# Kernel optimization log

Hardware: AMD Instinct MI355X
Metric: run time of the kernel (lower is better)

The kernel has to match this reference:

```python
import jax, jax.numpy as jnp
import numpy as np

B = 4096
FEATURES = 4608 + 4608 + 8 + 1  # 9225
LSTM = 512
R = FEATURES / LSTM
D1 = int(FEATURES / R ** (1.0 / 3.0))
D2 = int(FEATURES / R ** (2.0 / 3.0))
ACTION_SHAPES = (64, 64, 64, 64, 64, 64, 64, 64)


def setup_inputs() -> dict:
    key = jax.random.key(0)
    ks = jax.random.split(key, 32)
    s = 0.02
    inp = {
        "actualCanvasFeatures": jax.random.normal(ks[0], (B, 4608), jnp.float32),
        "objectiveCanvasFeatures": jax.random.normal(ks[1], (B, 4608), jnp.float32),
        "last_action": jax.random.uniform(ks[2], (B, 8), jnp.float32),
        "episode_percentage": 0,
        # encoder MLP
        "W1": jax.random.normal(ks[3], (FEATURES, D1), jnp.float32) * s,
        "b1": jnp.zeros((D1,), jnp.float32),
        "W2": jax.random.normal(ks[4], (D1, D2), jnp.float32) * s,
        "b2": jnp.zeros((D2,), jnp.float32),
        "W3": jax.random.normal(ks[5], (D2, LSTM), jnp.float32) * s,
        "b3": jnp.zeros((LSTM,), jnp.float32),
        # LSTM (torch gate order i,f,g,o)
        "Wih": jax.random.normal(ks[6], (4 * LSTM, LSTM), jnp.float32) * s,
        "Whh": jax.random.normal(ks[7], (4 * LSTM, LSTM), jnp.float32) * s,
        "bih": jnp.zeros((4 * LSTM,), jnp.float32),
        "bhh": jnp.zeros((4 * LSTM,), jnp.float32),
        "h0": jnp.zeros((B, LSTM), jnp.float32),
        "c0": jnp.zeros((B, LSTM), jnp.float32),
        # decoder
        "dW1": jax.random.normal(ks[8], (LSTM, LSTM // 2), jnp.float32) * s,
        "db1": jnp.zeros((LSTM // 2,), jnp.float32),
        "headWs": tuple(jax.random.normal(ks[9 + i], (LSTM // 2, a), jnp.float32) * s
                        for i, a in enumerate(ACTION_SHAPES)),
        "headbs": tuple(jnp.zeros((a,), jnp.float32) for a in ACTION_SHAPES),
        "dWo": jax.random.normal(ks[20], (LSTM + 1, LSTM), jnp.float32) * s,
        "dbo": jnp.zeros((LSTM,), jnp.float32),
    }
    return inp


def reference(actualCanvasFeatures, objectiveCanvasFeatures, last_action,
              episode_percentage, W1, b1, W2, b2, W3, b3, Wih, Whh, bih, bhh,
              h0, c0, dW1, db1, headWs, headbs, dWo, dbo):
    b = actualCanvasFeatures.shape[0]
    ep = jnp.full((b, 1), episode_percentage, dtype=jnp.float32)
    feats = jnp.concatenate(
        [actualCanvasFeatures, objectiveCanvasFeatures, last_action, ep], axis=1)
    # encoder MLP (dropout is eval-mode identity)
    x = jax.nn.relu(feats @ W1 + b1)
    x = jax.nn.relu(x @ W2 + b2)
    x = jax.nn.relu(x @ W3 + b3)
    # single-step LSTM cell, torch gate order i,f,g,o
    gates = x @ Wih.T + bih + h0 @ Whh.T + bhh
    i, f, g, o = jnp.split(gates, 4, axis=1)
    c = jax.nn.sigmoid(f) * c0 + jax.nn.sigmoid(i) * jnp.tanh(g)
    z = jax.nn.sigmoid(o) * jnp.tanh(c)  # seed
    key = jax.random.key(42)
    actions = []
    log_probabilities = jnp.zeros((b,), jnp.float32)
    entropy = jnp.float32(0.0)
    for Wk, bk in zip(headWs, headbs):
        z1 = jax.nn.relu(z @ dW1 + db1)
        logits = z1 @ Wk + bk
        logp = jax.nn.log_softmax(logits, axis=1)
        probs = jnp.exp(logp)
        key, sk = jax.random.split(key)
        act = jax.random.categorical(sk, logits, axis=1)  # [b] int
        actions.append(act.astype(jnp.float32))
        entropy = entropy + jnp.sum(-jnp.sum(probs * logp, axis=1))
        log_probabilities = log_probabilities + jnp.take_along_axis(
            logp, act[:, None], axis=1)[:, 0]
        z = jax.nn.relu(
            jnp.concatenate([z, act.astype(jnp.float32)[:, None]], axis=1) @ dWo + dbo)
    action = jnp.stack(actions, axis=1)  # [b, n_sub_actions]
    return action, entropy, log_probabilities
```

## Files before the change

### kernel.cpp

```cpp
#include <hip/hip_runtime.h>
#include <cstdint>
#include <cstring>

typedef _Float16 f16;
typedef _Float16 f16x8 __attribute__((ext_vector_type(8)));
typedef float f32x4 __attribute__((ext_vector_type(4)));

static constexpr int kPartitionable = 1;

__host__ __device__ inline void tf2x32(uint32_t k0, uint32_t k1,
                                       uint32_t x0, uint32_t x1,
                                       uint32_t& o0, uint32_t& o1) {
  uint32_t ks[3] = {k0, k1, k0 ^ k1 ^ 0x1BD11BDAu};
  uint32_t v0 = x0 + ks[0], v1 = x1 + ks[1];
  const int r0[4] = {13, 15, 26, 6};
  const int r1[4] = {17, 29, 16, 24};
  for (int g = 0; g < 5; ++g) {
    const int* rr = (g & 1) ? r1 : r0;
    for (int j = 0; j < 4; ++j) {
      v0 += v1;
      v1 = (v1 << rr[j]) | (v1 >> (32 - rr[j]));
      v1 ^= v0;
    }
    v0 += ks[(g + 1) % 3];
    v1 += ks[(g + 2) % 3] + (uint32_t)(g + 1);
  }
  o0 = v0; o1 = v1;
}

template <int BM, int BN>
__global__ __launch_bounds__(256, 2) void gemm_split(
    const f16* __restrict__ Ah, const f16* __restrict__ Al, int lda,
    const f16* __restrict__ Bh, const f16* __restrict__ Bl, int ldb,
    int K,
    const float* __restrict__ bias1, const float* __restrict__ bias2,
    int nReal, int relu, int writeF32,
    float* __restrict__ outF, f16* __restrict__ outH, f16* __restrict__ outL,
    int ldo) {
  constexpr int BK = 64;
  constexpr int TM = BM / 32;
  constexpr int TN = BN / 32;
  static_assert(BM == BN, "square tiles only");
  __shared__ f16 sAh[BM * BK];
  __shared__ f16 sAl[BM * BK];
  __shared__ f16 sBh[BN * BK];
  __shared__ f16 sBl[BN * BK];

  const int tid = threadIdx.x;
  const int wave = tid >> 6;
  const int lane = tid & 63;
  const int wm = wave & 1, wn = wave >> 1;
  const int m0 = blockIdx.x * BM;
  const int n0 = blockIdx.y * BN;

  f32x4 acc[TM][TN];
  const f32x4 zero = {0.f, 0.f, 0.f, 0.f};
#pragma unroll
  for (int i = 0; i < TM; ++i)
#pragma unroll
    for (int j = 0; j < TN; ++j) acc[i][j] = zero;

  const f16* src;
  f16* dst;
  int ld, base;
  if (wave == 0)      { src = Ah; dst = sAh; ld = lda; base = m0; }
  else if (wave == 1) { src = Al; dst = sAl; ld = lda; base = m0; }
  else if (wave == 2) { src = Bh; dst = sBh; ld = ldb; base = n0; }
  else                { src = Bl; dst = sBl; ld = ldb; base = n0; }
  constexpr int NITER = (BM * 8) / 64;

  for (int k0 = 0; k0 < K; k0 += BK) {
    __syncthreads();
#pragma unroll
    for (int j = 0; j < NITER; ++j) {
      int c = j * 64 + lane;
      int row = c >> 3, col = c & 7;
      const uint4* g = (const uint4*)(src + (size_t)(base + row) * ld + k0) + col;
      uint4 v = *g;
      ((uint4*)dst)[c] = v;
    }
    __syncthreads();
#pragma unroll
    for (int kk = 0; kk < BK; kk += 32) {
      const int fr = lane & 15;
      const int q8 = (lane >> 4) * 8;
      f16x8 aH[TM], aL[TM], bH[TN], bL[TN];
#pragma unroll
      for (int i = 0; i < TM; ++i) {
        int off = (wm * (BM / 2) + i * 16 + fr) * BK + kk + q8;
        aH[i] = *(const f16x8*)&sAh[off];
        aL[i] = *(const f16x8*)&sAl[off];
      }
#pragma unroll
      for (int j = 0; j < TN; ++j) {
        int off = (wn * (BN / 2) + j * 16 + fr) * BK + kk + q8;
        bH[j] = *(const f16x8*)&sBh[off];
        bL[j] = *(const f16x8*)&sBl[off];
      }
#pragma unroll
      for (int i = 0; i < TM; ++i)
#pragma unroll
        for (int j = 0; j < TN; ++j) {
          acc[i][j] = __builtin_amdgcn_mfma_f32_16x16x32_f16(aH[i], bH[j], acc[i][j], 0, 0, 0);
          acc[i][j] = __builtin_amdgcn_mfma_f32_16x16x32_f16(aH[i], bL[j], acc[i][j], 0, 0, 0);
          acc[i][j] = __builtin_amdgcn_mfma_f32_16x16x32_f16(aL[i], bH[j], acc[i][j], 0, 0, 0);
        }
    }
  }
  const int rq = lane >> 4, cl = lane & 15;
#pragma unroll
  for (int i = 0; i < TM; ++i)
#pragma unroll
    for (int j = 0; j < TN; ++j)
#pragma unroll
      for (int r = 0; r < 4; ++r) {
        int row = m0 + wm * (BM / 2) + i * 16 + rq * 4 + r;
        int col = n0 + wn * (BN / 2) + j * 16 + cl;
        float v = acc[i][j][r];
        if (col < nReal) {
          if (bias1) v += bias1[col];
          if (bias2) v += bias2[col];
          if (relu) v = fmaxf(v, 0.f);
        } else {
          v = 0.f;
        }
        size_t o = (size_t)row * ldo + col;
        if (writeF32) {
          outF[o] = v;
        } else {
          f16 h = (f16)v;
          outH[o] = h;
          outL[o] = (f16)(v - (float)h);
        }
      }
}

__global__ void conv_feats(const float* __restrict__ A, const float* __restrict__ O,
                           const float* __restrict__ LA, const int* __restrict__ EP,
                           f16* __restrict__ H, f16* __restrict__ L) {
  uint32_t idx = blockIdx.x * 256u + threadIdx.x;
  const uint32_t total = 4096u * 9280u;
  if (idx >= total) return;
  uint32_t b = idx / 9280u, c = idx - b * 9280u;
  float v;
  if (c < 4608u) v = A[(size_t)b * 4608 + c];
  else if (c < 9216u) v = O[(size_t)b * 4608 + (c - 4608u)];
  else if (c < 9224u) v = LA[(size_t)b * 8 + (c - 9216u)];
  else if (c == 9224u) v = (float)EP[0];
  else v = 0.f;
  f16 h = (f16)v;
  H[idx] = h;
  L[idx] = (f16)(v - (float)h);
}

__global__ void convT_kernel(const float* __restrict__ W, int Kreal, int Nreal,
                             f16* __restrict__ BtH, f16* __restrict__ BtL, int Kpad) {
  __shared__ float tile[32][33];
  int k0 = blockIdx.x * 32, n0 = blockIdx.y * 32;
  int tx = threadIdx.x, ty = threadIdx.y;
  for (int r = 0; r < 32; r += 8) {
    int k = k0 + ty + r, n = n0 + tx;
    float v = (k < Kreal && n < Nreal) ? W[(size_t)k * Nreal + n] : 0.f;
    tile[ty + r][tx] = v;
  }
  __syncthreads();
  for (int r = 0; r < 32; r += 8) {
    int n = n0 + ty + r, k = k0 + tx;
    float v = tile[tx][ty + r];
    size_t o = (size_t)n * Kpad + k;
    f16 h = (f16)v;
    BtH[o] = h;
    BtL[o] = (f16)(v - (float)h);
  }
}

__global__ void conv_lstmB(const float* __restrict__ Wih, const float* __restrict__ Whh,
                           f16* __restrict__ H, f16* __restrict__ L) {
  uint32_t idx = blockIdx.x * 256u + threadIdx.x;
  uint32_t n = idx >> 10, k = idx & 1023u;
  float v = (k < 512u) ? Wih[(size_t)n * 512 + k] : Whh[(size_t)n * 512 + (k - 512u)];
  f16 h = (f16)v;
  H[idx] = h;
  L[idx] = (f16)(v - (float)h);
}

__global__ void conv_h0(const float* __restrict__ h0, f16* __restrict__ H, f16* __restrict__ L) {
  uint32_t idx = blockIdx.x * 256u + threadIdx.x;
  uint32_t b = idx >> 9, j = idx & 511u;
  float v = h0[idx];
  size_t o = (size_t)b * 1024 + 512 + j;
  f16 h = (f16)v;
  H[o] = h;
  L[o] = (f16)(v - (float)h);
}

__global__ void lstm_pointwise(const float* __restrict__ gates, const float* __restrict__ c0,
                               f16* __restrict__ zH, f16* __restrict__ zL) {
  uint32_t idx = blockIdx.x * 256u + threadIdx.x;
  uint32_t b = idx >> 9, n = idx & 511u;
  const float* g = gates + (size_t)b * 2048;
  float gi = g[n], gf = g[512 + n], gg = g[1024 + n], go = g[1536 + n];
  float si = 1.f / (1.f + expf(-gi));
  float sf = 1.f / (1.f + expf(-gf));
  float so = 1.f / (1.f + expf(-go));
  float c = sf * c0[idx] + si * tanhf(gg);
  float z = so * tanhf(c);
  size_t o = (size_t)b * 576 + n;
  f16 h = (f16)z;
  zH[o] = h;
  zL[o] = (f16)(z - (float)h);
}

__global__ void init_ws(f16* zAH, f16* zAL, f16* zBH, f16* zBL,
                        float* wsLogp, float* wsEnt) {
  uint32_t idx = blockIdx.x * 256u + threadIdx.x;
  if (idx < 4096u * 63u) {
    uint32_t b = idx / 63u, c = 513u + idx - b * 63u;
    size_t o = (size_t)b * 576 + c;
    zAH[o] = (f16)0.f; zAL[o] = (f16)0.f; zBH[o] = (f16)0.f; zBL[o] = (f16)0.f;
  }
  if (idx < 4096u) wsLogp[idx] = 0.f;
  if (idx == 0) *wsEnt = 0.f;
}

__device__ inline double shfl_xor_dbl(double v, int m) {
  union { double d; int i[2]; } u;
  u.d = v;
  u.i[0] = __shfl_xor(u.i[0], m);
  u.i[1] = __shfl_xor(u.i[1], m);
  return u.d;
}

__global__ void sample_head(const float* __restrict__ logits,
                            uint32_t sk0, uint32_t sk1, int head, int partitionable,
                            float* __restrict__ outAct,
                            f16* __restrict__ zH, f16* __restrict__ zL,
                            float* __restrict__ wsLogp, float* __restrict__ wsEnt) {
  int wave = threadIdx.x >> 6, lane = threadIdx.x & 63;
  int b = blockIdx.x * 4 + wave;
  float l = logits[(size_t)b * 128 + lane];

  uint32_t i = (uint32_t)b * 64u + (uint32_t)lane;
  uint32_t bits;
  if (partitionable) {
    uint32_t o0, o1;
    tf2x32(sk0, sk1, 0u, i, o0, o1);
    bits = o0 ^ o1;
  } else {
    const uint32_t H = 131072u;
    uint32_t c0, c1, o0, o1;
    int pick;
    if (i < H) { c0 = i; c1 = i + H; pick = 0; }
    else       { c0 = i - H; c1 = i; pick = 1; }
    tf2x32(sk0, sk1, c0, c1, o0, o1);
    bits = pick ? o1 : o0;
  }
  uint32_t ub = (bits >> 9) | 0x3f800000u;
  float u;
  __builtin_memcpy(&u, &ub, 4);
  u -= 1.0f;
  if (u == 0.0f) u = 1.17549435e-38f;
  double gum = -log(-log((double)u));
  double s = (double)l + gum;

  int bi = lane;
  double bv = s;
#pragma unroll
  for (int off = 1; off < 64; off <<= 1) {
    double ov = shfl_xor_dbl(bv, off);
    int oi = __shfl_xor(bi, off);
    if (ov > bv || (ov == bv && oi < bi)) { bv = ov; bi = oi; }
  }
  int act = bi;

  float m = l;
#pragma unroll
  for (int off = 1; off < 64; off <<= 1) m = fmaxf(m, __shfl_xor(m, off));
  float e = expf(l - m);
  float S = e, D = e * l;
#pragma unroll
  for (int off = 1; off < 64; off <<= 1) {
    S += __shfl_xor(S, off);
    D += __shfl_xor(D, off);
  }
  float M = m + logf(S);
  float Hrow = M - D / S;
  float l_act = __shfl(l, act);

  if (lane == 0) {
    outAct[(size_t)b * 8 + head] = (float)act;
    wsLogp[b] += (l_act - M);
    size_t zo = (size_t)b * 576 + 512;
    zH[zo] = (f16)act;
    zL[zo] = (f16)0.f;
  }
  __shared__ float hs[4];
  if (lane == 0) hs[wave] = Hrow;
  __syncthreads();
  if (threadIdx.x == 0) atomicAdd(wsEnt, hs[0] + hs[1] + hs[2] + hs[3]);
}

__global__ void finalize_out(const float* __restrict__ wsEnt, const float* __restrict__ wsLogp,
                             float* __restrict__ out) {
  uint32_t idx = blockIdx.x * 256u + threadIdx.x;
  if (idx == 0) out[32768] = *wsEnt;
  if (idx < 4096u) out[32769 + idx] = wsLogp[idx];
}

extern "C" void kernel_launch(void* const* d_in, const int* in_sizes, int n_in,
                              void* d_out, int out_size, void* d_ws, size_t ws_size,
                              hipStream_t stream) {
  (void)in_sizes; (void)out_size; (void)ws_size;
  const float* actual = (const float*)d_in[0];
  const float* object = (const float*)d_in[1];
  const float* lastA = (const float*)d_in[2];
  const int* ep = (const int*)d_in[3];
  const float* W1 = (const float*)d_in[4];
  const float* b1 = (const float*)d_in[5];
  const float* W2 = (const float*)d_in[6];
  const float* b2 = (const float*)d_in[7];
  const float* W3 = (const float*)d_in[8];
  const float* b3 = (const float*)d_in[9];
  const float* Wih = (const float*)d_in[10];
  const float* Whh = (const float*)d_in[11];
  const float* bih = (const float*)d_in[12];
  const float* bhh = (const float*)d_in[13];
  const float* h0 = (const float*)d_in[14];
  const float* c0 = (const float*)d_in[15];
  const float* dW1 = (const float*)d_in[16];
  const float* db1 = (const float*)d_in[17];
  const float* headW[8];
  const float* headb[8];
  const float *dWo, *dbo;
  if (n_in >= 36) {
    for (int h = 0; h < 8; ++h) headW[h] = (const float*)d_in[18 + h];
    for (int h = 0; h < 8; ++h) headb[h] = (const float*)d_in[26 + h];
    dWo = (const float*)d_in[34];
    dbo = (const float*)d_in[35];
  } else {
    const float* hw = (const float*)d_in[18];
    const float* hb = (const float*)d_in[19];
    for (int h = 0; h < 8; ++h) { headW[h] = hw + (size_t)h * 256 * 64; headb[h] = hb + (size_t)h * 64; }
    dWo = (const float*)d_in[20];
    dbo = (const float*)d_in[21];
  }

  constexpr int Bq = 4096;
  constexpr int K1 = 9280, N1 = 3584, N1r = 3518;
  constexpr int K2 = 3584, N2 = 1408, N2r = 1342;
  constexpr int K3 = 1408, N3 = 512;
  constexpr int KL = 1024, NL = 2048;
  constexpr int KD1 = 512, ND1 = 256;
  constexpr int KH = 256, NHp = 128;
  constexpr int KDO = 576, NDO = 512;

  uint8_t* w = (uint8_t*)d_ws;
  size_t off = 0;
  auto alloc = [&](size_t bytes) -> void* {
    off = (off + 1023) & ~(size_t)1023;
    void* p = w + off;
    off += bytes;
    return p;
  };
  f16* A1h = (f16*)alloc((size_t)Bq * K1 * 2);
  f16* A1l = (f16*)alloc((size_t)Bq * K1 * 2);
  size_t fixedReuseEnd = off;
  f16* Bt1h = (f16*)alloc((size_t)N1 * K1 * 2);
  f16* Bt1l = (f16*)alloc((size_t)N1 * K1 * 2);
  f16* x1h = (f16*)alloc((size_t)Bq * K2 * 2);
  f16* x1l = (f16*)alloc((size_t)Bq * K2 * 2);
  f16* Bt2h = (f16*)alloc((size_t)N2 * K2 * 2);
  f16* Bt2l = (f16*)alloc((size_t)N2 * K2 * 2);
  size_t poff = 0;
  auto palloc = [&](size_t bytes) -> void* {
    poff = (poff + 1023) & ~(size_t)1023;
    void* p = w + poff;
    poff += bytes;
    return p;
  };
  f16* x2h = (f16*)palloc((size_t)Bq * K3 * 2);
  f16* x2l = (f16*)palloc((size_t)Bq * K3 * 2);
  f16* Bt3h = (f16*)palloc((size_t)N3 * K3 * 2);
  f16* Bt3l = (f16*)palloc((size_t)N3 * K3 * 2);
  f16* ALh = (f16*)palloc((size_t)Bq * KL * 2);
  f16* ALl = (f16*)palloc((size_t)Bq * KL * 2);
  f16* BLh = (f16*)palloc((size_t)NL * KL * 2);
  f16* BLl = (f16*)palloc((size_t)NL * KL * 2);
  float* gates = (float*)palloc((size_t)Bq * NL * 4);
  f16* zAH = (f16*)palloc((size_t)Bq * 576 * 2);
  f16* zAL = (f16*)palloc((size_t)Bq * 576 * 2);
  f16* zBH = (f16*)palloc((size_t)Bq * 576 * 2);
  f16* zBL = (f16*)palloc((size_t)Bq * 576 * 2);
  f16* Btd1h = (f16*)palloc((size_t)ND1 * KD1 * 2);
  f16* Btd1l = (f16*)palloc((size_t)ND1 * KD1 * 2);
  f16* z1h = (f16*)palloc((size_t)Bq * ND1 * 2);
  f16* z1l = (f16*)palloc((size_t)Bq * ND1 * 2);
  f16* Bthh = (f16*)palloc((size_t)8 * NHp * KH * 2);
  f16* Bthl = (f16*)palloc((size_t)8 * NHp * KH * 2);
  float* logitsF = (float*)palloc((size_t)Bq * 128 * 4);
  f16* Btdoh = (f16*)palloc((size_t)NDO * KDO * 2);
  f16* Btdol = (f16*)palloc((size_t)NDO * KDO * 2);
  float* wsLogp = (float*)palloc((size_t)Bq * 4);
  float* wsEnt = (float*)palloc(64);
  (void)fixedReuseEnd;

  uint32_t k0 = 0u, k1 = 42u;
  uint32_t sk[8][2];
  for (int h = 0; h < 8; ++h) {
    if (kPartitionable) {
      uint32_t a0, a1, b0v, b1v;
      tf2x32(k0, k1, 0u, 0u, a0, a1);
      tf2x32(k0, k1, 0u, 1u, b0v, b1v);
      sk[h][0] = b0v; sk[h][1] = b1v;
      k0 = a0; k1 = a1;
    } else {
      uint32_t a0, a1, b0v, b1v;
      tf2x32(k0, k1, 0u, 2u, a0, a1);
      tf2x32(k0, k1, 1u, 3u, b0v, b1v);
      sk[h][0] = a1; sk[h][1] = b1v;
      k0 = a0; k1 = b0v;
    }
  }

  dim3 blk(256);
  dim3 tblk(32, 8);

  conv_feats<<<(4096u * 9280u + 255) / 256, blk, 0, stream>>>(actual, object, lastA, ep, A1h, A1l);
  convT_kernel<<<dim3(K1 / 32, N1 / 32), tblk, 0, stream>>>(W1, 9225, 3518, Bt1h, Bt1l, K1);
  convT_kernel<<<dim3(K2 / 32, N2 / 32), tblk, 0, stream>>>(W2, 3518, 1342, Bt2h, Bt2l, K2);

  gemm_split<128, 128><<<dim3(Bq / 128, N1 / 128), blk, 0, stream>>>(
      A1h, A1l, K1, Bt1h, Bt1l, K1, K1, b1, nullptr, N1r, 1, 0, nullptr, x1h, x1l, K2);

  init_ws<<<(4096u * 63u + 255) / 256, blk, 0, stream>>>(zAH, zAL, zBH, zBL, wsLogp, wsEnt);
  convT_kernel<<<dim3(K3 / 32, N3 / 32), tblk, 0, stream>>>(W3, 1342, 512, Bt3h, Bt3l, K3);
  conv_lstmB<<<(2048u * 1024u) / 256, blk, 0, stream>>>(Wih, Whh, BLh, BLl);
  conv_h0<<<(4096u * 512u) / 256, blk, 0, stream>>>(h0, ALh, ALl);
  convT_kernel<<<dim3(KD1 / 32, ND1 / 32), tblk, 0, stream>>>(dW1, 512, 256, Btd1h, Btd1l, KD1);
  convT_kernel<<<dim3(KDO / 32, NDO / 32), tblk, 0, stream>>>(dWo, 513, 512, Btdoh, Btdol, KDO);
  for (int h = 0; h < 8; ++h)
    convT_kernel<<<dim3(KH / 32, NHp / 32), tblk, 0, stream>>>(
        headW[h], 256, 64, Bthh + (size_t)h * NHp * KH, Bthl + (size_t)h * NHp * KH, KH);

  gemm_split<128, 128><<<dim3(Bq / 128, N2 / 128), blk, 0, stream>>>(
      x1h, x1l, K2, Bt2h, Bt2l, K2, K2, b2, nullptr, N2r, 1, 0, nullptr, x2h, x2l, K3);
  gemm_split<128, 128><<<dim3(Bq / 128, N3 / 128), blk, 0, stream>>>(
      x2h, x2l, K3, Bt3h, Bt3l, K3, K3, b3, nullptr, N3, 1, 0, nullptr, ALh, ALl, KL);
  gemm_split<128, 128><<<dim3(Bq / 128, NL / 128), blk, 0, stream>>>(
      ALh, ALl, KL, BLh, BLl, KL, KL, bih, bhh, NL, 0, 1, gates, nullptr, nullptr, NL);
  lstm_pointwise<<<(4096u * 512u) / 256, blk, 0, stream>>>(gates, c0, zAH, zAL);

  for (int h = 0; h < 8; ++h) {
    f16* curH = (h & 1) ? zBH : zAH;
    f16* curL = (h & 1) ? zBL : zAL;
    f16* nxtH = (h & 1) ? zAH : zBH;
    f16* nxtL = (h & 1) ? zAL : zBL;
    gemm_split<64, 64><<<dim3(Bq / 64, ND1 / 64), blk, 0, stream>>>(
        curH, curL, 576, Btd1h, Btd1l, KD1, KD1, db1, nullptr, ND1, 1, 0, nullptr, z1h, z1l, ND1);
    gemm_split<64, 64><<<dim3(Bq / 64, NHp / 64), blk, 0, stream>>>(
        z1h, z1l, ND1, Bthh + (size_t)h * NHp * KH, Bthl + (size_t)h * NHp * KH, KH, KH,
        headb[h], nullptr, 64, 0, 1, logitsF, nullptr, nullptr, 128);
    sample_head<<<Bq / 4, blk, 0, stream>>>(logitsF, sk[h][0], sk[h][1], h, kPartitionable,
                                            (float*)d_out, curH, curL, wsLogp, wsEnt);
    gemm_split<64, 64><<<dim3(Bq / 64, NDO / 64), blk, 0, stream>>>(
        curH, curL, 576, Btdoh, Btdol, KDO, KDO, dbo, nullptr, NDO, 1, 0, nullptr, nxtH, nxtL, 576);
  }
  finalize_out<<<(4097 + 255) / 256, blk, 0, stream>>>(wsEnt, wsLogp, (float*)d_out);
}
```

Baseline: 2.311 ms.

## Use direct global-to-LDS loads with XOR-swizzled layouts and trim head padding

Replaces the register-staged global→LDS copy in the split-fp16 GEMM with the global_load_lds builtin. All producer kernels now write operands in an XOR-swizzled column order so the LDS reads avoid bank conflicts. The head weights are no longer padded to 128 columns, which halves the head GEMM grid, and the eight per-head transpose launches are merged into one launch. Every writer of GEMM operands must apply the same swizzle, so a missed site would silently corrupt results.

```diff
diff --git a/kernel.cpp b/kernel.cpp
--- a/kernel.cpp
+++ b/kernel.cpp
@@ -7,6 +7,18 @@
 typedef float f32x4 __attribute__((ext_vector_type(4)));
 
 static constexpr int kPartitionable = 1;
+
+struct Ptr8 { const float* p[8]; };
+
+__device__ __host__ __forceinline__ int swz(int r, int k) {
+  return k ^ ((r & 7) << 3);
+}
+
+__device__ __forceinline__ void gload16(const void* g, void* l) {
+  __builtin_amdgcn_global_load_lds(
+      (const __attribute__((address_space(1))) unsigned int*)g,
+      (__attribute__((address_space(3))) unsigned int*)l, 16, 0, 0);
+}
 
 __host__ __device__ inline void tf2x32(uint32_t k0, uint32_t k1,
                                        uint32_t x0, uint32_t x1,
@@ -67,33 +79,32 @@
   else if (wave == 1) { src = Al; dst = sAl; ld = lda; base = m0; }
   else if (wave == 2) { src = Bh; dst = sBh; ld = ldb; base = n0; }
   else                { src = Bl; dst = sBl; ld = ldb; base = n0; }
-  constexpr int NITER = (BM * 8) / 64;
+  constexpr int NITER = BM / 8;
+  const f16* gbase = src + (size_t)(base + (lane >> 3)) * ld + (lane & 7) * 8;
+
+  const int fr = lane & 15;
+  const int q8 = (lane >> 4) * 8;
+  const int sw = (fr & 7) << 3;
 
   for (int k0 = 0; k0 < K; k0 += BK) {
     __syncthreads();
 #pragma unroll
-    for (int j = 0; j < NITER; ++j) {
-      int c = j * 64 + lane;
-      int row = c >> 3, col = c & 7;
-      const uint4* g = (const uint4*)(src + (size_t)(base + row) * ld + k0) + col;
-      uint4 v = *g;
-      ((uint4*)dst)[c] = v;
-    }
+    for (int j = 0; j < NITER; ++j)
+      gload16(gbase + (size_t)(j * 8) * ld + k0, dst + j * 512);
     __syncthreads();
 #pragma unroll
     for (int kk = 0; kk < BK; kk += 32) {
-      const int fr = lane & 15;
-      const int q8 = (lane >> 4) * 8;
+      const int kf = (kk + q8) ^ sw;
       f16x8 aH[TM], aL[TM], bH[TN], bL[TN];
 #pragma unroll
       for (int i = 0; i < TM; ++i) {
-        int off = (wm * (BM / 2) + i * 16 + fr) * BK + kk + q8;
+        int off = (wm * (BM / 2) + i * 16 + fr) * BK + kf;
         aH[i] = *(const f16x8*)&sAh[off];
         aL[i] = *(const f16x8*)&sAl[off];
       }
 #pragma unroll
       for (int j = 0; j < TN; ++j) {
-        int off = (wn * (BN / 2) + j * 16 + fr) * BK + kk + q8;
+        int off = (wn * (BN / 2) + j * 16 + fr) * BK + kf;
         bH[j] = *(const f16x8*)&sBh[off];
         bL[j] = *(const f16x8*)&sBl[off];
       }
@@ -124,10 +135,10 @@
         } else {
           v = 0.f;
         }
-        size_t o = (size_t)row * ldo + col;
         if (writeF32) {
-          outF[o] = v;
+          outF[(size_t)row * ldo + col] = v;
         } else {
+          size_t o = (size_t)row * ldo + swz(row, col);
           f16 h = (f16)v;
           outH[o] = h;
           outL[o] = (f16)(v - (float)h);
@@ -148,9 +159,10 @@
   else if (c < 9224u) v = LA[(size_t)b * 8 + (c - 9216u)];
   else if (c == 9224u) v = (float)EP[0];
   else v = 0.f;
+  size_t o = (size_t)b * 9280 + swz((int)b, (int)c);
   f16 h = (f16)v;
-  H[idx] = h;
-  L[idx] = (f16)(v - (float)h);
+  H[o] = h;
+  L[o] = (f16)(v - (float)h);
 }
 
 __global__ void convT_kernel(const float* __restrict__ W, int Kreal, int Nreal,
@@ -167,10 +179,33 @@
   for (int r = 0; r < 32; r += 8) {
     int n = n0 + ty + r, k = k0 + tx;
     float v = tile[tx][ty + r];
-    size_t o = (size_t)n * Kpad + k;
+    size_t o = (size_t)n * Kpad + swz(n, k);
     f16 h = (f16)v;
     BtH[o] = h;
     BtL[o] = (f16)(v - (float)h);
+  }
+}
+
+__global__ void convT_heads(Ptr8 ws, f16* __restrict__ BtH, f16* __restrict__ BtL) {
+  __shared__ float tile[32][33];
+  int h = blockIdx.z;
+  const float* W = ws.p[h];
+  int k0 = blockIdx.x * 32, n0 = blockIdx.y * 32;
+  int tx = threadIdx.x, ty = threadIdx.y;
+  for (int r = 0; r < 32; r += 8) {
+    int k = k0 + ty + r, n = n0 + tx;
+    float v = (k < 256 && n < 64) ? W[(size_t)k * 64 + n] : 0.f;
+    tile[ty + r][tx] = v;
+  }
+  __syncthreads();
+  size_t base = (size_t)h * 64 * 256;
+  for (int r = 0; r < 32; r += 8) {
+    int n = n0 + ty + r, k = k0 + tx;
+    float v = tile[tx][ty + r];
+    size_t o = base + (size_t)n * 256 + swz(n, k);
+    f16 hh = (f16)v;
+    BtH[o] = hh;
+    BtL[o] = (f16)(v - (float)hh);
   }
 }
 
@@ -179,16 +214,17 @@
   uint32_t idx = blockIdx.x * 256u + threadIdx.x;
   uint32_t n = idx >> 10, k = idx & 1023u;
   float v = (k < 512u) ? Wih[(size_t)n * 512 + k] : Whh[(size_t)n * 512 + (k - 512u)];
+  size_t o = (size_t)n * 1024 + swz((int)n, (int)k);
   f16 h = (f16)v;
-  H[idx] = h;
-  L[idx] = (f16)(v - (float)h);
+  H[o] = h;
+  L[o] = (f16)(v - (float)h);
 }
 
 __global__ void conv_h0(const float* __restrict__ h0, f16* __restrict__ H, f16* __restrict__ L) {
   uint32_t idx = blockIdx.x * 256u + threadIdx.x;
   uint32_t b = idx >> 9, j = idx & 511u;
   float v = h0[idx];
-  size_t o = (size_t)b * 1024 + 512 + j;
+  size_t o = (size_t)b * 1024 + swz((int)b, (int)(512 + j));
   f16 h = (f16)v;
   H[o] = h;
   L[o] = (f16)(v - (float)h);
@@ -205,7 +241,7 @@
   float so = 1.f / (1.f + expf(-go));
   float c = sf * c0[idx] + si * tanhf(gg);
   float z = so * tanhf(c);
-  size_t o = (size_t)b * 576 + n;
+  size_t o = (size_t)b * 576 + swz((int)b, (int)n);
   f16 h = (f16)z;
   zH[o] = h;
   zL[o] = (f16)(z - (float)h);
@@ -216,7 +252,7 @@
   uint32_t idx = blockIdx.x * 256u + threadIdx.x;
   if (idx < 4096u * 63u) {
     uint32_t b = idx / 63u, c = 513u + idx - b * 63u;
-    size_t o = (size_t)b * 576 + c;
+    size_t o = (size_t)b * 576 + swz((int)b, (int)c);
     zAH[o] = (f16)0.f; zAL[o] = (f16)0.f; zBH[o] = (f16)0.f; zBL[o] = (f16)0.f;
   }
   if (idx < 4096u) wsLogp[idx] = 0.f;
@@ -238,7 +274,7 @@
                             float* __restrict__ wsLogp, float* __restrict__ wsEnt) {
   int wave = threadIdx.x >> 6, lane = threadIdx.x & 63;
   int b = blockIdx.x * 4 + wave;
-  float l = logits[(size_t)b * 128 + lane];
+  float l = logits[(size_t)b * 64 + lane];
 
   uint32_t i = (uint32_t)b * 64u + (uint32_t)lane;
   uint32_t bits;
@@ -290,7 +326,7 @@
   if (lane == 0) {
     outAct[(size_t)b * 8 + head] = (float)act;
     wsLogp[b] += (l_act - M);
-    size_t zo = (size_t)b * 576 + 512;
+    size_t zo = (size_t)b * 576 + swz(b, 512);
     zH[zo] = (f16)act;
     zL[zo] = (f16)0.f;
   }
@@ -339,8 +375,8 @@
     dbo = (const float*)d_in[35];
   } else {
     const float* hw = (const float*)d_in[18];
-    const float* hb = (const float*)d_in[19];
-    for (int h = 0; h < 8; ++h) { headW[h] = hw + (size_t)h * 256 * 64; headb[h] = hb + (size_t)h * 64; }
+    const float* hbp = (const float*)d_in[19];
+    for (int h = 0; h < 8; ++h) { headW[h] = hw + (size_t)h * 256 * 64; headb[h] = hbp + (size_t)h * 64; }
     dWo = (const float*)d_in[20];
     dbo = (const float*)d_in[21];
   }
@@ -351,7 +387,7 @@
   constexpr int K3 = 1408, N3 = 512;
   constexpr int KL = 1024, NL = 2048;
   constexpr int KD1 = 512, ND1 = 256;
-  constexpr int KH = 256, NHp = 128;
+  constexpr int KH = 256;
   constexpr int KDO = 576, NDO = 512;
 
   uint8_t* w = (uint8_t*)d_ws;
@@ -364,7 +400,6 @@
   };
   f16* A1h = (f16*)alloc((size_t)Bq * K1 * 2);
   f16* A1l = (f16*)alloc((size_t)Bq * K1 * 2);
-  size_t fixedReuseEnd = off;
   f16* Bt1h = (f16*)alloc((size_t)N1 * K1 * 2);
   f16* Bt1l = (f16*)alloc((size_t)N1 * K1 * 2);
   f16* x1h = (f16*)alloc((size_t)Bq * K2 * 2);
@@ -395,14 +430,13 @@
   f16* Btd1l = (f16*)palloc((size_t)ND1 * KD1 * 2);
   f16* z1h = (f16*)palloc((size_t)Bq * ND1 * 2);
   f16* z1l = (f16*)palloc((size_t)Bq * ND1 * 2);
-  f16* Bthh = (f16*)palloc((size_t)8 * NHp * KH * 2);
-  f16* Bthl = (f16*)palloc((size_t)8 * NHp * KH * 2);
-  float* logitsF = (float*)palloc((size_t)Bq * 128 * 4);
+  f16* Bthh = (f16*)palloc((size_t)8 * 64 * KH * 2);
+  f16* Bthl = (f16*)palloc((size_t)8 * 64 * KH * 2);
+  float* logitsF = (float*)palloc((size_t)Bq * 64 * 4);
   f16* Btdoh = (f16*)palloc((size_t)NDO * KDO * 2);
   f16* Btdol = (f16*)palloc((size_t)NDO * KDO * 2);
   float* wsLogp = (float*)palloc((size_t)Bq * 4);
   float* wsEnt = (float*)palloc(64);
-  (void)fixedReuseEnd;
 
   uint32_t k0 = 0u, k1 = 42u;
   uint32_t sk[8][2];
@@ -421,6 +455,8 @@
       k0 = a0; k1 = b0v;
     }
   }
+  Ptr8 hws;
+  for (int h = 0; h < 8; ++h) hws.p[h] = headW[h];
 
   dim3 blk(256);
   dim3 tblk(32, 8);
@@ -438,9 +474,7 @@
   conv_h0<<<(4096u * 512u) / 256, blk, 0, stream>>>(h0, ALh, ALl);
   convT_kernel<<<dim3(KD1 / 32, ND1 / 32), tblk, 0, stream>>>(dW1, 512, 256, Btd1h, Btd1l, KD1);
   convT_kernel<<<dim3(KDO / 32, NDO / 32), tblk, 0, stream>>>(dWo, 513, 512, Btdoh, Btdol, KDO);
-  for (int h = 0; h < 8; ++h)
-    convT_kernel<<<dim3(KH / 32, NHp / 32), tblk, 0, stream>>>(
-        headW[h], 256, 64, Bthh + (size_t)h * NHp * KH, Bthl + (size_t)h * NHp * KH, KH);
+  convT_heads<<<dim3(KH / 32, 2, 8), tblk, 0, stream>>>(hws, Bthh, Bthl);
 
   gemm_split<128, 128><<<dim3(Bq / 128, N2 / 128), blk, 0, stream>>>(
       x1h, x1l, K2, Bt2h, Bt2l, K2, K2, b2, nullptr, N2r, 1, 0, nullptr, x2h, x2l, K3);
@@ -457,9 +491,9 @@
     f16* nxtL = (h & 1) ? zAL : zBL;
     gemm_split<64, 64><<<dim3(Bq / 64, ND1 / 64), blk, 0, stream>>>(
         curH, curL, 576, Btd1h, Btd1l, KD1, KD1, db1, nullptr, ND1, 1, 0, nullptr, z1h, z1l, ND1);
-    gemm_split<64, 64><<<dim3(Bq / 64, NHp / 64), blk, 0, stream>>>(
-        z1h, z1l, ND1, Bthh + (size_t)h * NHp * KH, Bthl + (size_t)h * NHp * KH, KH, KH,
-        headb[h], nullptr, 64, 0, 1, logitsF, nullptr, nullptr, 128);
+    gemm_split<64, 64><<<dim3(Bq / 64, 1), blk, 0, stream>>>(
+        z1h, z1l, ND1, Bthh + (size_t)h * 64 * KH, Bthl + (size_t)h * 64 * KH, KH, KH,
+        headb[h], nullptr, 64, 0, 1, logitsF, nullptr, nullptr, 64);
     sample_head<<<Bq / 4, blk, 0, stream>>>(logitsF, sk[h][0], sk[h][1], h, kPartitionable,
                                             (float*)d_out, curH, curL, wsLogp, wsEnt);
     gemm_split<64, 64><<<dim3(Bq / 64, NDO / 64), blk, 0, stream>>>(
```

Result: faster. 1.874 ms (-18.9%).
